# Kernel tuning notes

Measured on AMD Instinct MI355X. Metric: run time of the kernel, lower is better.

Reference implementation:

```python
import jax, jax.numpy as jnp
import numpy as np


def quat_to_rotmat(q):
    """COLMAP-convention qvec2rotmat, vectorized. q: [N,4] = (w, x, y, z).
    Note: matches the repo's qvec2rotmat, which does NOT normalize q."""
    w, x, y, z = q[:, 0], q[:, 1], q[:, 2], q[:, 3]
    R = jnp.stack([
        1 - 2 * y * y - 2 * z * z, 2 * x * y - 2 * w * z, 2 * x * z + 2 * w * y,
        2 * x * y + 2 * w * z, 1 - 2 * x * x - 2 * z * z, 2 * y * z - 2 * w * x,
        2 * x * z - 2 * w * y, 2 * y * z + 2 * w * x, 1 - 2 * x * x - 2 * y * y,
    ], axis=-1)  # [N, 9]
    return R.reshape(-1, 3, 3)


def setup_inputs() -> dict:
    key = jax.random.key(0)
    k1, k2 = jax.random.split(key)
    N = 4_000_000
    # Match the module's init: near-identity quaternions and unit scales + tiny noise.
    quaternions = jnp.tile(jnp.array([0., 0., 0., 1.], jnp.float32), (N, 1)) \
        + jax.random.normal(k1, (N, 4), jnp.float32) * 1e-6
    scales = jnp.ones((N, 3), jnp.float32) + jax.random.normal(k2, (N, 3), jnp.float32) * 1e-6
    return {"quaternions": quaternions, "scales": scales}


def reference(quaternions, scales):
    # covariance = (R @ diag(s)) @ (R @ diag(s))^T
    R = quat_to_rotmat(quaternions)                # [N,3,3]
    M = R * scales[:, None, :]                     # R @ diag(s), column scaling
    cov = jnp.einsum('nik,njk->nij', M, M)         # M @ M^T, symmetric [N,3,3]
    return cov
```

## Files before the change

### kernel.cpp

```cpp
#include <hip/hip_runtime.h>


__global__ __launch_bounds__(256) void gaussian_cov_kernel(
    const float4* __restrict__ quat,
    const float*  __restrict__ scales,
    float*        __restrict__ out,
    int N) {
    __shared__ float lds[256 * 9];

    const int t = threadIdx.x;
    const int i = blockIdx.x * 256 + t;

    if (i < N) {
        const float4 q = quat[i];
        const float w = q.x, x = q.y, y = q.z, z = q.w;
        const float sx = scales[3 * i + 0];
        const float sy = scales[3 * i + 1];
        const float sz = scales[3 * i + 2];

        const float xx = 2.0f * x * x, yy = 2.0f * y * y, zz = 2.0f * z * z;
        const float xy = 2.0f * x * y, xz = 2.0f * x * z, yz = 2.0f * y * z;
        const float wx = 2.0f * w * x, wy = 2.0f * w * y, wz = 2.0f * w * z;

        const float R00 = 1.0f - yy - zz, R01 = xy - wz, R02 = xz + wy;
        const float R10 = xy + wz, R11 = 1.0f - xx - zz, R12 = yz - wx;
        const float R20 = xz - wy, R21 = yz + wx, R22 = 1.0f - xx - yy;

        const float s2x = sx * sx, s2y = sy * sy, s2z = sz * sz;

        const float c00 = R00 * R00 * s2x + R01 * R01 * s2y + R02 * R02 * s2z;
        const float c01 = R00 * R10 * s2x + R01 * R11 * s2y + R02 * R12 * s2z;
        const float c02 = R00 * R20 * s2x + R01 * R21 * s2y + R02 * R22 * s2z;
        const float c11 = R10 * R10 * s2x + R11 * R11 * s2y + R12 * R12 * s2z;
        const float c12 = R10 * R20 * s2x + R11 * R21 * s2y + R12 * R22 * s2z;
        const float c22 = R20 * R20 * s2x + R21 * R21 * s2y + R22 * R22 * s2z;

        float* l = &lds[t * 9];
        l[0] = c00; l[1] = c01; l[2] = c02;
        l[3] = c01; l[4] = c11; l[5] = c12;
        l[6] = c02; l[7] = c12; l[8] = c22;
    }

    __syncthreads();

    const int base = blockIdx.x * (256 * 9);
    const int total = N * 9;
#pragma unroll
    for (int r = 0; r < 9; ++r) {
        const int idx = r * 256 + t;
        if (base + idx < total) {
            out[base + idx] = lds[idx];
        }
    }
}

extern "C" void kernel_launch(void* const* d_in, const int* in_sizes, int n_in,
                              void* d_out, int out_size, void* d_ws, size_t ws_size,
                              hipStream_t stream) {
    const float4* quat   = (const float4*)d_in[0];
    const float*  scales = (const float*)d_in[1];
    float*        out    = (float*)d_out;
    const int N = in_sizes[0] / 4;
    const int blocks = (N + 255) / 256;
    gaussian_cov_kernel<<<blocks, 256, 0, stream>>>(quat, scales, out, N);
}
```

Baseline: 225.4 us.

## Stage scales through LDS with vector loads and use nontemporal float4 output stores

Scales are loaded cooperatively as 16-byte vectors into shared memory instead of three strided scalar loads per thread. The covariance output is written from LDS with float4 nontemporal stores for full blocks, replacing nine scalar stores per thread. The aim is fewer, wider memory transactions and less cache pollution on a bandwidth-bound kernel. It adds a second barrier and a small LDS buffer, and keeps a scalar fallback for the tail block.

```diff
diff --git a/kernel.cpp b/kernel.cpp
--- a/kernel.cpp
+++ b/kernel.cpp
@@ -1,22 +1,46 @@
 #include <hip/hip_runtime.h>
 
 
-__global__ __launch_bounds__(256) void gaussian_cov_kernel(
+constexpr int TPB = 256;
+
+typedef float f32x4 __attribute__((ext_vector_type(4)));
+
+__global__ __launch_bounds__(TPB) void gaussian_cov_kernel(
     const float4* __restrict__ quat,
     const float*  __restrict__ scales,
     float*        __restrict__ out,
     int N) {
-    __shared__ float lds[256 * 9];
+    __shared__ __align__(16) float sOut[TPB * 9];
+    __shared__ __align__(16) float sScl[TPB * 3];
 
-    const int t = threadIdx.x;
-    const int i = blockIdx.x * 256 + t;
+    const int t   = threadIdx.x;
+    const int blk = blockIdx.x;
+    const int i   = blk * TPB + t;
+
+    const int sclBase = blk * (TPB * 3);
+    const int sclTot  = N * 3;
+    if (t < (TPB * 3) / 4) {
+        const int f = sclBase + t * 4;
+        if (f + 4 <= sclTot) {
+            reinterpret_cast<f32x4*>(sScl)[t] =
+                reinterpret_cast<const f32x4*>(scales + sclBase)[t];
+        } else {
+#pragma unroll
+            for (int k = 0; k < 4; ++k)
+                if (f + k < sclTot) sScl[t * 4 + k] = scales[f + k];
+        }
+    }
+
+    float4 q = make_float4(0.f, 0.f, 0.f, 0.f);
+    if (i < N) q = quat[i];
+
+    __syncthreads();
 
     if (i < N) {
-        const float4 q = quat[i];
         const float w = q.x, x = q.y, y = q.z, z = q.w;
-        const float sx = scales[3 * i + 0];
-        const float sy = scales[3 * i + 1];
-        const float sz = scales[3 * i + 2];
+        const float sx = sScl[t * 3 + 0];
+        const float sy = sScl[t * 3 + 1];
+        const float sz = sScl[t * 3 + 2];
 
         const float xx = 2.0f * x * x, yy = 2.0f * y * y, zz = 2.0f * z * z;
         const float xy = 2.0f * x * y, xz = 2.0f * x * z, yz = 2.0f * y * z;
@@ -35,7 +59,7 @@
         const float c12 = R10 * R20 * s2x + R11 * R21 * s2y + R12 * R22 * s2z;
         const float c22 = R20 * R20 * s2x + R21 * R21 * s2y + R22 * R22 * s2z;
 
-        float* l = &lds[t * 9];
+        float* l = &sOut[t * 9];
         l[0] = c00; l[1] = c01; l[2] = c02;
         l[3] = c01; l[4] = c11; l[5] = c12;
         l[6] = c02; l[7] = c12; l[8] = c22;
@@ -43,13 +67,21 @@
 
     __syncthreads();
 
-    const int base = blockIdx.x * (256 * 9);
-    const int total = N * 9;
+    const int outBase = blk * (TPB * 9);
+    const int total   = N * 9;
+    if (outBase + TPB * 9 <= total) {
+        const f32x4* src = reinterpret_cast<const f32x4*>(sOut);
+        f32x4*       dst = reinterpret_cast<f32x4*>(out + outBase);
+        __builtin_nontemporal_store(src[t],         &dst[t]);
+        __builtin_nontemporal_store(src[TPB + t],   &dst[TPB + t]);
+        if (t < 64) {
+            __builtin_nontemporal_store(src[2 * TPB + t], &dst[2 * TPB + t]);
+        }
+    } else {
 #pragma unroll
-    for (int r = 0; r < 9; ++r) {
-        const int idx = r * 256 + t;
-        if (base + idx < total) {
-            out[base + idx] = lds[idx];
+        for (int r = 0; r < 9; ++r) {
+            const int idx = r * TPB + t;
+            if (outBase + idx < total) out[outBase + idx] = sOut[idx];
         }
     }
 }
@@ -61,6 +93,6 @@
     const float*  scales = (const float*)d_in[1];
     float*        out    = (float*)d_out;
     const int N = in_sizes[0] / 4;
-    const int blocks = (N + 255) / 256;
-    gaussian_cov_kernel<<<blocks, 256, 0, stream>>>(quat, scales, out, N);
+    const int blocks = (N + TPB - 1) / TPB;
+    gaussian_cov_kernel<<<blocks, TPB, 0, stream>>>(quat, scales, out, N);
 }
```

New measurement: 223.1 us. No clear change (-1.0%).

## Stage scales and outputs per wavefront with vector nontemporal I/O in grid-stride loop

Applied to the files above, without the earlier changes.

Switches to per-wavefront groups of 64 elements in a grid-stride loop capped at 2048 blocks. Scales are loaded as coalesced 16-byte nontemporal vectors into per-wave LDS, which removes the strided 3-float loads. Outputs go out as 16-byte nontemporal stores from per-wave LDS, and the block-wide __syncthreads is dropped. The exchange through LDS inside a wave now relies on lockstep wavefront execution with no explicit barrier, which is a correctness risk if the compiler reorders the LDS accesses.

```diff
diff --git a/kernel.cpp b/kernel.cpp
--- a/kernel.cpp
+++ b/kernel.cpp
@@ -1,55 +1,88 @@
 #include <hip/hip_runtime.h>
 
 
-__global__ __launch_bounds__(256) void gaussian_cov_kernel(
-    const float4* __restrict__ quat,
-    const float*  __restrict__ scales,
-    float*        __restrict__ out,
+constexpr int TPB = 256;
+constexpr int NW  = TPB / 64;
+
+typedef float f32x4 __attribute__((ext_vector_type(4)));
+
+__global__ __launch_bounds__(TPB) void gaussian_cov_kernel(
+    const f32x4* __restrict__ quat,
+    const float* __restrict__ scales,
+    float*       __restrict__ out,
     int N) {
-    __shared__ float lds[256 * 9];
+    __shared__ __align__(16) float sOut[NW][64 * 9];
+    __shared__ __align__(16) float sScl[NW][64 * 3];
 
-    const int t = threadIdx.x;
-    const int i = blockIdx.x * 256 + t;
+    const int t    = threadIdx.x;
+    const int lane = t & 63;
+    const int w    = t >> 6;
 
-    if (i < N) {
-        const float4 q = quat[i];
-        const float w = q.x, x = q.y, y = q.z, z = q.w;
-        const float sx = scales[3 * i + 0];
-        const float sy = scales[3 * i + 1];
-        const float sz = scales[3 * i + 2];
+    const int nGroups = (N + 63) >> 6;
+    const int gStride = gridDim.x * NW;
 
-        const float xx = 2.0f * x * x, yy = 2.0f * y * y, zz = 2.0f * z * z;
-        const float xy = 2.0f * x * y, xz = 2.0f * x * z, yz = 2.0f * y * z;
-        const float wx = 2.0f * w * x, wy = 2.0f * w * y, wz = 2.0f * w * z;
+    for (int g = blockIdx.x * NW + w; g < nGroups; g += gStride) {
+        const int base = g << 6;
+        const int i    = base + lane;
 
-        const float R00 = 1.0f - yy - zz, R01 = xy - wz, R02 = xz + wy;
-        const float R10 = xy + wz, R11 = 1.0f - xx - zz, R12 = yz - wx;
-        const float R20 = xz - wy, R21 = yz + wx, R22 = 1.0f - xx - yy;
+        if (lane < 48) {
+            const int f = base * 3 + lane * 4;
+            if (f + 4 <= N * 3) {
+                reinterpret_cast<f32x4*>(sScl[w])[lane] =
+                    __builtin_nontemporal_load(
+                        reinterpret_cast<const f32x4*>(scales + base * 3) + lane);
+            } else {
+#pragma unroll
+                for (int k = 0; k < 4; ++k)
+                    if (f + k < N * 3) sScl[w][lane * 4 + k] = scales[f + k];
+            }
+        }
 
-        const float s2x = sx * sx, s2y = sy * sy, s2z = sz * sz;
+        f32x4 q = 0.0f;
+        if (i < N) q = __builtin_nontemporal_load(quat + i);
 
-        const float c00 = R00 * R00 * s2x + R01 * R01 * s2y + R02 * R02 * s2z;
-        const float c01 = R00 * R10 * s2x + R01 * R11 * s2y + R02 * R12 * s2z;
-        const float c02 = R00 * R20 * s2x + R01 * R21 * s2y + R02 * R22 * s2z;
-        const float c11 = R10 * R10 * s2x + R11 * R11 * s2y + R12 * R12 * s2z;
-        const float c12 = R10 * R20 * s2x + R11 * R21 * s2y + R12 * R22 * s2z;
-        const float c22 = R20 * R20 * s2x + R21 * R21 * s2y + R22 * R22 * s2z;
+        if (i < N) {
+            const float qw = q.x, qx = q.y, qy = q.z, qz = q.w;
+            const float sx = sScl[w][lane * 3 + 0];
+            const float sy = sScl[w][lane * 3 + 1];
+            const float sz = sScl[w][lane * 3 + 2];
 
-        float* l = &lds[t * 9];
-        l[0] = c00; l[1] = c01; l[2] = c02;
-        l[3] = c01; l[4] = c11; l[5] = c12;
-        l[6] = c02; l[7] = c12; l[8] = c22;
-    }
+            const float xx = 2.0f * qx * qx, yy = 2.0f * qy * qy, zz = 2.0f * qz * qz;
+            const float xy = 2.0f * qx * qy, xz = 2.0f * qx * qz, yz = 2.0f * qy * qz;
+            const float wx = 2.0f * qw * qx, wy = 2.0f * qw * qy, wz = 2.0f * qw * qz;
 
-    __syncthreads();
+            const float R00 = 1.0f - yy - zz, R01 = xy - wz, R02 = xz + wy;
+            const float R10 = xy + wz, R11 = 1.0f - xx - zz, R12 = yz - wx;
+            const float R20 = xz - wy, R21 = yz + wx, R22 = 1.0f - xx - yy;
 
-    const int base = blockIdx.x * (256 * 9);
-    const int total = N * 9;
+            const float s2x = sx * sx, s2y = sy * sy, s2z = sz * sz;
+
+            const float c00 = R00 * R00 * s2x + R01 * R01 * s2y + R02 * R02 * s2z;
+            const float c01 = R00 * R10 * s2x + R01 * R11 * s2y + R02 * R12 * s2z;
+            const float c02 = R00 * R20 * s2x + R01 * R21 * s2y + R02 * R22 * s2z;
+            const float c11 = R10 * R10 * s2x + R11 * R11 * s2y + R12 * R12 * s2z;
+            const float c12 = R10 * R20 * s2x + R11 * R21 * s2y + R12 * R22 * s2z;
+            const float c22 = R20 * R20 * s2x + R21 * R21 * s2y + R22 * R22 * s2z;
+
+            float* l = &sOut[w][lane * 9];
+            l[0] = c00; l[1] = c01; l[2] = c02;
+            l[3] = c01; l[4] = c11; l[5] = c12;
+            l[6] = c02; l[7] = c12; l[8] = c22;
+        }
+
+        if (base + 64 <= N) {
+            const f32x4* src = reinterpret_cast<const f32x4*>(sOut[w]);
+            f32x4*       dst = reinterpret_cast<f32x4*>(out) + (size_t)144 * g;
+            __builtin_nontemporal_store(src[lane],      dst + lane);
+            __builtin_nontemporal_store(src[64 + lane], dst + 64 + lane);
+            if (lane < 16)
+                __builtin_nontemporal_store(src[128 + lane], dst + 128 + lane);
+        } else {
 #pragma unroll
-    for (int r = 0; r < 9; ++r) {
-        const int idx = r * 256 + t;
-        if (base + idx < total) {
-            out[base + idx] = lds[idx];
+            for (int r = 0; r < 9; ++r) {
+                const int idx = r * 64 + lane;
+                if (base * 9 + idx < N * 9) out[base * 9 + idx] = sOut[w][idx];
+            }
         }
     }
 }
@@ -57,10 +90,12 @@
 extern "C" void kernel_launch(void* const* d_in, const int* in_sizes, int n_in,
                               void* d_out, int out_size, void* d_ws, size_t ws_size,
                               hipStream_t stream) {
-    const float4* quat   = (const float4*)d_in[0];
-    const float*  scales = (const float*)d_in[1];
-    float*        out    = (float*)d_out;
+    const f32x4* quat   = (const f32x4*)d_in[0];
+    const float* scales = (const float*)d_in[1];
+    float*       out    = (float*)d_out;
     const int N = in_sizes[0] / 4;
-    const int blocks = (N + 255) / 256;
-    gaussian_cov_kernel<<<blocks, 256, 0, stream>>>(quat, scales, out, N);
+    const int nGroups = (N + 63) / 64;
+    int blocks = (nGroups + NW - 1) / NW;
+    if (blocks > 2048) blocks = 2048;
+    gaussian_cov_kernel<<<blocks, TPB, 0, stream>>>(quat, scales, out, N);
 }
```

After: 218.5 us. 1.03x faster.
